# Optimization experiments

Hardware: AMD Instinct MI355X
Metric: run time of the kernel (lower is better)

## Reference

```python
import jax, jax.numpy as jnp
import numpy as np

D_MODEL = 256
N_HEADS = 8
B, S = 8, 2048
TEMP = jnp.sqrt(jnp.float32(D_MODEL))  # ScaledDotProductAttention(temperature=d_model) -> sqrt(d_model)
NEG = jnp.float32(-1e9)


def setup_inputs() -> dict:
    key = jax.random.key(0)
    ks = jax.random.split(key, 12)
    dh = D_MODEL * N_HEADS
    sc_in = 1.0 / np.sqrt(D_MODEL)
    sc_out = 1.0 / np.sqrt(dh)
    return {
        "query": jax.random.normal(ks[0], (B, S, D_MODEL), jnp.float32),
        "key": jax.random.normal(ks[1], (B, S, D_MODEL), jnp.float32),
        "value": jax.random.normal(ks[2], (B, S, D_MODEL), jnp.float32),
        "mask": jax.random.bernoulli(ks[3], 0.9, (B, S)),
        "Wq": jax.random.normal(ks[4], (D_MODEL, dh), jnp.float32) * sc_in,
        "bq": jnp.zeros((dh,), jnp.float32),
        "Wk": jax.random.normal(ks[5], (D_MODEL, dh), jnp.float32) * sc_in,
        "bk": jnp.zeros((dh,), jnp.float32),
        "Wv": jax.random.normal(ks[6], (D_MODEL, dh), jnp.float32) * sc_in,
        "bv": jnp.zeros((dh,), jnp.float32),
        "Wo": jax.random.normal(ks[7], (dh, D_MODEL), jnp.float32) * sc_out,
        "bo": jnp.zeros((D_MODEL,), jnp.float32),
    }


def reference(query, key, value, mask, Wq, bq, Wk, bk, Wv, bv, Wo, bo):
    nb = query.shape[0]
    # projections: (B,S,d) @ (d, d*H) -> view (B,S,H,d)
    q = (query @ Wq + bq).reshape(nb, -1, N_HEADS, D_MODEL)
    k = (key @ Wk + bk).reshape(nb, -1, N_HEADS, D_MODEL)
    v = (value @ Wv + bv).reshape(nb, -1, N_HEADS, D_MODEL)
    # torch.matmul on (B,S,H,d): batched over (B,S) -> per-position HxH attention
    attn = jnp.einsum('bshd,bsgd->bshg', q, k) / TEMP
    m = mask[:, :, None, None]  # (B,S,1,1) broadcast, as in mask.view(B,-1,1,1)
    attn = jnp.where(m, attn, NEG)
    attn = jax.nn.softmax(attn, axis=-1)  # dropout p=0 -> identity
    x = jnp.einsum('bshg,bsgd->bshd', attn, v)  # (B,S,H,d)
    # x.transpose(1,2).contiguous().view(B,-1,d*H)
    x = jnp.transpose(x, (0, 2, 1, 3)).reshape(nb, -1, D_MODEL * N_HEADS)
    return x @ Wo + bo
```

## Files before the change

kernel.cpp:

```cpp
#include <hip/hip_runtime.h>
#include <hip/hip_bf16.h>

typedef __hip_bfloat16 bf16;
typedef short bf16x8 __attribute__((ext_vector_type(8)));
typedef float f32x4 __attribute__((ext_vector_type(4)));

#define MFMA16(a,b,c) __builtin_amdgcn_mfma_f32_16x16x32_bf16(a,b,c,0,0,0)

__device__ __forceinline__ unsigned short f2us(float x){
    union{__hip_bfloat16 h; unsigned short u;} c; c.h = __float2bfloat16(x); return c.u;
}
__device__ __forceinline__ float us2f(unsigned short u){
    union{unsigned short u; __hip_bfloat16 h;} c; c.u = u; return __bfloat162float(c.h);
}
__device__ __forceinline__ uint4 pack8(float4 a, float4 b){
    union{unsigned short us[8]; uint4 v;} p;
    p.us[0]=f2us(a.x); p.us[1]=f2us(a.y); p.us[2]=f2us(a.z); p.us[3]=f2us(a.w);
    p.us[4]=f2us(b.x); p.us[5]=f2us(b.y); p.us[6]=f2us(b.z); p.us[7]=f2us(b.w);
    return p.v;
}

__global__ __launch_bounds__(256) void prep_kernel(
    const float* __restrict__ Wq, const float* __restrict__ Wk,
    const float* __restrict__ Wv, const float* __restrict__ bq,
    const float* __restrict__ bk, const float* __restrict__ bv,
    const float* __restrict__ Wo,
    bf16* __restrict__ WqT, bf16* __restrict__ WkT, bf16* __restrict__ WvT,
    float* __restrict__ bqp, float* __restrict__ bkp, float* __restrict__ bvp,
    bf16* __restrict__ WoT)
{
    __shared__ float T[64][68];
    const int tid = threadIdx.x, bx = blockIdx.x;
    if (bx < 384) {
        const int mat = bx / 128, rem = bx % 128;
        const int c0 = (rem >> 5) * 64, n0 = (rem & 31) * 64;
        const float* W = (mat == 0) ? Wq : (mat == 1) ? Wk : Wv;
        bf16* WT = (mat == 0) ? WqT : (mat == 1) ? WkT : WvT;
        #pragma unroll
        for (int it = 0; it < 4; ++it) {
            int pp = tid + (it << 8);
            int cl = pp >> 4, n4 = (pp & 15) * 4;
            float4 f = *(const float4*)(W + (size_t)(c0 + cl) * 2048 + n0 + n4);
            T[cl][n4] = f.x; T[cl][n4+1] = f.y; T[cl][n4+2] = f.z; T[cl][n4+3] = f.w;
        }
        __syncthreads();
        const int h = n0 >> 8, d0 = n0 & 255;
        #pragma unroll
        for (int it = 0; it < 2; ++it) {
            int pp = tid + (it << 8);
            int j = pp >> 3, g = pp & 7;
            union{unsigned short us[8]; uint4 v;} pk;
            #pragma unroll
            for (int u = 0; u < 8; ++u) pk.us[u] = f2us(T[g*8+u][j]);
            *(uint4*)(WT + (size_t)((d0 + j) * 8 + h) * 256 + c0 + g * 8) = pk.v;
        }
    } else if (bx < 387) {
        const int mat = bx - 384;
        const float* src = (mat == 0) ? bq : (mat == 1) ? bk : bv;
        float* dst = (mat == 0) ? bqp : (mat == 1) ? bkp : bvp;
        for (int n = tid; n < 2048; n += 256)
            dst[(n & 255) * 8 + (n >> 8)] = src[n];
    } else {
        const int idx = bx - 387;
        const int k0 = (idx >> 2) * 64, c0 = (idx & 3) * 64;
        #pragma unroll
        for (int it = 0; it < 4; ++it) {
            int pp = tid + (it << 8);
            int kl = pp >> 4, c4 = (pp & 15) * 4;
            float4 f = *(const float4*)(Wo + (size_t)(k0 + kl) * 256 + c0 + c4);
            T[kl][c4] = f.x; T[kl][c4+1] = f.y; T[kl][c4+2] = f.z; T[kl][c4+3] = f.w;
        }
        __syncthreads();
        #pragma unroll
        for (int it = 0; it < 2; ++it) {
            int pp = tid + (it << 8);
            int j = pp >> 3, g = pp & 7;
            union{unsigned short us[8]; uint4 v;} pk;
            #pragma unroll
            for (int u = 0; u < 8; ++u) pk.us[u] = f2us(T[g*8+u][j]);
            *(uint4*)(WoT + (size_t)(c0 + j) * 2048 + k0 + g * 8) = pk.v;
        }
    }
}

__global__ __launch_bounds__(512, 2) void qkav_kernel(
    const float* __restrict__ Qin, const float* __restrict__ Kin,
    const float* __restrict__ Vin, const int* __restrict__ mask,
    const bf16* __restrict__ WqT, const bf16* __restrict__ WkT,
    const bf16* __restrict__ WvT,
    const float* __restrict__ bqp, const float* __restrict__ bkp,
    const float* __restrict__ bvp,
    const bf16* __restrict__ WoT, const float* __restrict__ bo,
    float* __restrict__ Out)
{
    __shared__ __align__(16) char smem[147456];
    char* const Xq = smem;
    char* const Xk = smem + 32768;
    char* const QT = smem + 65536;
    char* const KT = smem + 106496;
    float* const RED  = (float*)smem;
    float* const WLDS = (float*)(smem + 106496);
    char* const Xv  = smem;
    char* const VT0 = smem + 32768;
    char* const VT1 = smem + 50176;
    char* const xS0 = smem + 67584;
    char* const xS1 = smem + 83968;

    const int tid  = threadIdx.x;
    const int wid  = tid >> 6, lane = tid & 63;
    const int quad = lane >> 4, l15 = lane & 15;
    const int tok0 = blockIdx.x * 64;
    const int t6   = tid & 63, dg = tid >> 6;

    #pragma unroll
    for (int it = 0; it < 4; ++it) {
        int pp = tid + (it << 9);
        int row = pp >> 5, g = pp & 31;
        const float* s = Qin + (size_t)(tok0 + row) * 256 + g * 8;
        *(uint4*)(Xq + row * 512 + ((g ^ (row & 7)) << 4)) =
            pack8(*(const float4*)s, *(const float4*)(s + 4));
        s = Kin + (size_t)(tok0 + row) * 256 + g * 8;
        *(uint4*)(Xk + row * 512 + ((g ^ (row & 7)) << 4)) =
            pack8(*(const float4*)s, *(const float4*)(s + 4));
    }
    __syncthreads();

    f32x4 sacc[4];
    #pragma unroll
    for (int p = 0; p < 4; ++p)
        #pragma unroll
        for (int i = 0; i < 4; ++i) sacc[p][i] = 0.f;

    for (int Cp = 0; Cp < 8; ++Cp) {
        f32x4 accq[4][2], acck[4][2];
        #pragma unroll
        for (int mt = 0; mt < 4; ++mt)
            #pragma unroll
            for (int nt = 0; nt < 2; ++nt)
                #pragma unroll
                for (int i = 0; i < 4; ++i) { accq[mt][nt][i] = 0.f; acck[mt][nt][i] = 0.f; }
        #pragma unroll
        for (int Ks = 0; Ks < 8; ++Ks) {
            bf16x8 bq[2], bk[2];
            #pragma unroll
            for (int nt = 0; nt < 2; ++nt) {
                const size_t boff =
                    (size_t)(Cp * 256 + wid * 32 + nt * 16 + l15) * 256 + Ks * 32 + quad * 8;
                bq[nt] = *(const bf16x8*)(WqT + boff);
                bk[nt] = *(const bf16x8*)(WkT + boff);
            }
            #pragma unroll
            for (int mt = 0; mt < 4; ++mt) {
                int row = mt * 16 + l15;
                int G = (Ks * 4 + quad) ^ (row & 7);
                bf16x8 aq = *(const bf16x8*)(Xq + row * 512 + (G << 4));
                bf16x8 ak = *(const bf16x8*)(Xk + row * 512 + (G << 4));
                #pragma unroll
                for (int nt = 0; nt < 2; ++nt) {
                    accq[mt][nt] = MFMA16(aq, bq[nt], accq[mt][nt]);
                    acck[mt][nt] = MFMA16(ak, bk[nt], acck[mt][nt]);
                }
            }
        }
        #pragma unroll
        for (int nt = 0; nt < 2; ++nt) {
            const int p2 = wid * 32 + nt * 16 + l15;
            const int rowoff = p2 * 160 + ((p2 >> 6) & 3) * 8;
            const float biq = bqp[Cp * 256 + p2];
            const float bik = bkp[Cp * 256 + p2];
            #pragma unroll
            for (int mt = 0; mt < 4; ++mt) {
                int t0 = mt * 16 + quad * 4;
                union{unsigned short us[4]; uint2 v;} pq, pk;
                #pragma unroll
                for (int i = 0; i < 4; ++i) {
                    pq.us[i] = f2us(accq[mt][nt][i] + biq);
                    pk.us[i] = f2us(acck[mt][nt][i] + bik);
                }
                *(uint2*)(QT + rowoff + t0 * 2) = pq.v;
                *(uint2*)(KT + rowoff + t0 * 2) = pk.v;
            }
        }
        __syncthreads();
        #pragma unroll
        for (int pp2 = 0; pp2 < 4; ++pp2) {
            int tq = 2 * (wid * 4 + pp2) + (l15 >> 3);
            union{unsigned short us[8]; bf16x8 v;} Aq, Bk;
            #pragma unroll
            for (int j = 0; j < 8; ++j) {
                int p2 = (quad * 8 + j) * 8 + (l15 & 7);
                int off = p2 * 160 + ((p2 >> 6) & 3) * 8 + tq * 2;
                Aq.us[j] = *(const unsigned short*)(QT + off);
                Bk.us[j] = *(const unsigned short*)(KT + off);
            }
            sacc[pp2] = MFMA16(Aq.v, Bk.v, sacc[pp2]);
        }
        __syncthreads();
    }

    if ((quad >> 1) == (l15 >> 3)) {
        #pragma unroll
        for (int pp2 = 0; pp2 < 4; ++pp2) {
            int tl = (wid * 4 + pp2) * 2 + (l15 >> 3);
            #pragma unroll
            for (int i = 0; i < 4; ++i)
                RED[tl * 68 + ((quad & 1) * 4 + i) * 8 + (l15 & 7)] = sacc[pp2][i];
        }
    }
    __syncthreads();
    {
        const int tl = tid >> 3, hh = tid & 7;
        const int mk = mask[tok0 + tl];
        const float* r = RED + tl * 68 + hh * 8;
        float m = r[0];
        #pragma unroll
        for (int g = 1; g < 8; ++g) m = fmaxf(m, r[g]);
        float e[8], sum = 0.f;
        #pragma unroll
        for (int g = 0; g < 8; ++g) { e[g] = __expf((r[g] - m) * 0.0625f); sum += e[g]; }
        float inv = 1.f / sum;
        float o[8];
        #pragma unroll
        for (int g = 0; g < 8; ++g) o[g] = mk ? e[g] * inv : 0.125f;
        float* wp = WLDS + tl * 68 + hh * 8;
        *(float4*)wp = make_float4(o[0], o[1], o[2], o[3]);
        *(float4*)(wp + 4) = make_float4(o[4], o[5], o[6], o[7]);
    }
    __syncthreads();

    float wv[64];
    {
        const float* wl = WLDS + t6 * 68;
        #pragma unroll
        for (int i = 0; i < 16; ++i) {
            float4 f = *(const float4*)(wl + i * 4);
            wv[i*4] = f.x; wv[i*4+1] = f.y; wv[i*4+2] = f.z; wv[i*4+3] = f.w;
        }
    }
    #pragma unroll
    for (int it = 0; it < 4; ++it) {
        int pp = tid + (it << 9);
        int row = pp >> 5, g = pp & 31;
        const float* s = Vin + (size_t)(tok0 + row) * 256 + g * 8;
        *(uint4*)(Xv + row * 512 + ((g ^ (row & 7)) << 4)) =
            pack8(*(const float4*)s, *(const float4*)(s + 4));
    }
    __syncthreads();

    const int pll = wid * 16 + l15;

    f32x4 oacc[4][2];
    #pragma unroll
    for (int mt = 0; mt < 4; ++mt)
        #pragma unroll
        for (int nt = 0; nt < 2; ++nt)
            #pragma unroll
            for (int i = 0; i < 4; ++i) oacc[mt][nt][i] = 0.f;

    for (int p = 0; p < 18; ++p) {
        char* const VTw = (p & 1) ? VT1 : VT0;
        char* const VTr = (p & 1) ? VT0 : VT1;
        char* const xSw = (p & 1) ? xS0 : xS1;
        char* const xSr = (p & 1) ? xS1 : xS0;

        if (p < 16) {
            const int C = p;
            f32x4 acc[4];
            #pragma unroll
            for (int mt = 0; mt < 4; ++mt)
                #pragma unroll
                for (int i = 0; i < 4; ++i) acc[mt][i] = 0.f;
            #pragma unroll
            for (int Ks = 0; Ks < 8; ++Ks) {
                bf16x8 b = *(const bf16x8*)(WvT + (size_t)(C * 128 + pll) * 256 + Ks * 32 + quad * 8);
                #pragma unroll
                for (int mt = 0; mt < 4; ++mt) {
                    int row = mt * 16 + l15;
                    int G = (Ks * 4 + quad) ^ (row & 7);
                    bf16x8 a = *(const bf16x8*)(Xv + row * 512 + (G << 4));
                    acc[mt] = MFMA16(a, b, acc[mt]);
                }
            }
            const float biv = bvp[C * 128 + pll];
            #pragma unroll
            for (int mt = 0; mt < 4; ++mt) {
                int t0 = mt * 16 + quad * 4;
                union{unsigned short us[4]; uint2 v;} pk;
                #pragma unroll
                for (int i = 0; i < 4; ++i) pk.us[i] = f2us(acc[mt][i] + biv);
                *(uint2*)(VTw + pll * 136 + t0 * 2) = pk.v;
            }
        }

        if (p >= 1 && p <= 16) {
            #pragma unroll
            for (int dd = 0; dd < 2; ++dd) {
                int d = dg * 2 + dd;
                float vv[8];
                #pragma unroll
                for (int g = 0; g < 8; ++g)
                    vv[g] = us2f(*(const unsigned short*)(VTr + (d * 8 + g) * 136 + t6 * 2));
                #pragma unroll
                for (int h = 0; h < 8; ++h) {
                    float x = 0.f;
                    #pragma unroll
                    for (int g = 0; g < 8; ++g) x = fmaf(wv[h * 8 + g], vv[g], x);
                    int u = (h * 2 + (d >> 3)) ^ (t6 & 15);
                    *(unsigned short*)(xSw + t6 * 256 + u * 16 + (d & 7) * 2) = f2us(x);
                }
            }
        }

        if (p >= 2) {
            const int C = p - 2;
            #pragma unroll
            for (int m = 0; m < 4; ++m) {
                const int j  = 2 * m + (quad >> 1);
                const int k0 = j * 256 + C * 16 + (quad & 1) * 8;
                bf16x8 bfr[2];
                #pragma unroll
                for (int nt = 0; nt < 2; ++nt) {
                    int c = wid * 32 + nt * 16 + l15;
                    bfr[nt] = *(const bf16x8*)(WoT + (size_t)c * 2048 + k0);
                }
                #pragma unroll
                for (int mt = 0; mt < 4; ++mt) {
                    int h = mt * 2 + (l15 >> 3);
                    int t = (l15 & 7) * 8 + j;
                    int u = (h * 2 + (quad & 1)) ^ (t & 15);
                    bf16x8 afr = *(const bf16x8*)(xSr + t * 256 + u * 16);
                    #pragma unroll
                    for (int nt = 0; nt < 2; ++nt)
                        oacc[mt][nt] = MFMA16(afr, bfr[nt], oacc[mt][nt]);
                }
            }
        }

        __syncthreads();
    }

    const int b = tok0 >> 11, sg0 = (tok0 & 2047) >> 3;
    #pragma unroll
    for (int nt = 0; nt < 2; ++nt) {
        int c = wid * 32 + nt * 16 + l15;
        float bias = bo[c];
        #pragma unroll
        for (int mt = 0; mt < 4; ++mt) {
            #pragma unroll
            for (int i = 0; i < 4; ++i) {
                int rr = mt * 16 + quad * 4 + i;
                int h = rr >> 3, sgl = rr & 7;
                size_t r = ((size_t)b << 11) + h * 256 + sg0 + sgl;
                Out[r * 256 + c] = oacc[mt][nt][i] + bias;
            }
        }
    }
}

extern "C" void kernel_launch(void* const* d_in, const int* in_sizes, int n_in,
                              void* d_out, int out_size, void* d_ws, size_t ws_size,
                              hipStream_t stream) {
    const float* query = (const float*)d_in[0];
    const float* key   = (const float*)d_in[1];
    const float* value = (const float*)d_in[2];
    const int*   mask  = (const int*)  d_in[3];
    const float* Wq = (const float*)d_in[4];  const float* bq = (const float*)d_in[5];
    const float* Wk = (const float*)d_in[6];  const float* bk = (const float*)d_in[7];
    const float* Wv = (const float*)d_in[8];  const float* bv = (const float*)d_in[9];
    const float* Wo = (const float*)d_in[10]; const float* bo = (const float*)d_in[11];

    char* ws = (char*)d_ws;
    bf16*  WoT = (bf16*)ws;
    bf16*  WqT = (bf16*)(ws + 1048576);
    bf16*  WkT = (bf16*)(ws + 2097152);
    bf16*  WvT = (bf16*)(ws + 3145728);
    float* bqp = (float*)(ws + 4194304);
    float* bkp = (float*)(ws + 4202496);
    float* bvp = (float*)(ws + 4210688);

    prep_kernel<<<515, 256, 0, stream>>>(
        Wq, Wk, Wv, bq, bk, bv, Wo, WqT, WkT, WvT, bqp, bkp, bvp, WoT);
    qkav_kernel<<<256, 512, 0, stream>>>(
        query, key, value, mask, WqT, WkT, WvT, bqp, bkp, bvp, WoT, bo,
        (float*)d_out);
}
```

Measured before the change: 262.7 us.

## Prefetch next-chunk weight fragments and V input into registers; use lightweight barriers

Software-prefetches the first three K-slices of the Wq/Wk and Wv weight fragments for the next chunk into registers while the current chunk computes. The V input loads are issued early, before the softmax phase, to hide global latency. __syncthreads is replaced with an inline-asm barrier that only waits on LDS counters, so outstanding global loads are not drained at each barrier. This adds register pressure (extra bf16x8 and float4 arrays), which may reduce occupancy or cause spills.

```diff
diff --git a/kernel.cpp b/kernel.cpp
--- a/kernel.cpp
+++ b/kernel.cpp
@@ -6,6 +6,8 @@
 typedef float f32x4 __attribute__((ext_vector_type(4)));
 
 #define MFMA16(a,b,c) __builtin_amdgcn_mfma_f32_16x16x32_bf16(a,b,c,0,0,0)
+
+#define BARRIER() asm volatile("s_waitcnt lgkmcnt(0)\n\ts_barrier" ::: "memory")
 
 __device__ __forceinline__ unsigned short f2us(float x){
     union{__hip_bfloat16 h; unsigned short u;} c; c.h = __float2bfloat16(x); return c.u;
@@ -112,6 +114,17 @@
     const int tok0 = blockIdx.x * 64;
     const int t6   = tid & 63, dg = tid >> 6;
 
+    bf16x8 pbq[2][3], pbk[2][3];
+    #pragma unroll
+    for (int nt = 0; nt < 2; ++nt)
+        #pragma unroll
+        for (int Ks = 0; Ks < 3; ++Ks) {
+            const size_t boff =
+                (size_t)(wid * 32 + nt * 16 + l15) * 256 + Ks * 32 + quad * 8;
+            pbq[nt][Ks] = *(const bf16x8*)(WqT + boff);
+            pbk[nt][Ks] = *(const bf16x8*)(WkT + boff);
+        }
+
     #pragma unroll
     for (int it = 0; it < 4; ++it) {
         int pp = tid + (it << 9);
@@ -123,7 +136,7 @@
         *(uint4*)(Xk + row * 512 + ((g ^ (row & 7)) << 4)) =
             pack8(*(const float4*)s, *(const float4*)(s + 4));
     }
-    __syncthreads();
+    BARRIER();
 
     f32x4 sacc[4];
     #pragma unroll
@@ -144,10 +157,15 @@
             bf16x8 bq[2], bk[2];
             #pragma unroll
             for (int nt = 0; nt < 2; ++nt) {
-                const size_t boff =
-                    (size_t)(Cp * 256 + wid * 32 + nt * 16 + l15) * 256 + Ks * 32 + quad * 8;
-                bq[nt] = *(const bf16x8*)(WqT + boff);
-                bk[nt] = *(const bf16x8*)(WkT + boff);
+                if (Ks < 3) {
+                    bq[nt] = pbq[nt][Ks];
+                    bk[nt] = pbk[nt][Ks];
+                } else {
+                    const size_t boff =
+                        (size_t)(Cp * 256 + wid * 32 + nt * 16 + l15) * 256 + Ks * 32 + quad * 8;
+                    bq[nt] = *(const bf16x8*)(WqT + boff);
+                    bk[nt] = *(const bf16x8*)(WkT + boff);
+                }
             }
             #pragma unroll
             for (int mt = 0; mt < 4; ++mt) {
@@ -162,6 +180,17 @@
                 }
             }
         }
+        if (Cp < 7) {
+            #pragma unroll
+            for (int nt = 0; nt < 2; ++nt)
+                #pragma unroll
+                for (int Ks = 0; Ks < 3; ++Ks) {
+                    const size_t boff =
+                        (size_t)((Cp + 1) * 256 + wid * 32 + nt * 16 + l15) * 256 + Ks * 32 + quad * 8;
+                    pbq[nt][Ks] = *(const bf16x8*)(WqT + boff);
+                    pbk[nt][Ks] = *(const bf16x8*)(WkT + boff);
+                }
+        }
         #pragma unroll
         for (int nt = 0; nt < 2; ++nt) {
             const int p2 = wid * 32 + nt * 16 + l15;
@@ -181,7 +210,7 @@
                 *(uint2*)(KT + rowoff + t0 * 2) = pk.v;
             }
         }
-        __syncthreads();
+        BARRIER();
         #pragma unroll
         for (int pp2 = 0; pp2 < 4; ++pp2) {
             int tq = 2 * (wid * 4 + pp2) + (l15 >> 3);
@@ -195,8 +224,23 @@
             }
             sacc[pp2] = MFMA16(Aq.v, Bk.v, sacc[pp2]);
         }
-        __syncthreads();
-    }
+        BARRIER();
+    }
+
+    float4 xvA[4], xvB[4];
+    #pragma unroll
+    for (int it = 0; it < 4; ++it) {
+        int pp = tid + (it << 9);
+        int row = pp >> 5, g = pp & 31;
+        const float* s = Vin + (size_t)(tok0 + row) * 256 + g * 8;
+        xvA[it] = *(const float4*)s;
+        xvB[it] = *(const float4*)(s + 4);
+    }
+    const int pll = wid * 16 + l15;
+    bf16x8 pv[3];
+    #pragma unroll
+    for (int Ks = 0; Ks < 3; ++Ks)
+        pv[Ks] = *(const bf16x8*)(WvT + (size_t)pll * 256 + Ks * 32 + quad * 8);
 
     if ((quad >> 1) == (l15 >> 3)) {
         #pragma unroll
@@ -207,7 +251,7 @@
                 RED[tl * 68 + ((quad & 1) * 4 + i) * 8 + (l15 & 7)] = sacc[pp2][i];
         }
     }
-    __syncthreads();
+    BARRIER();
     {
         const int tl = tid >> 3, hh = tid & 7;
         const int mk = mask[tok0 + tl];
@@ -226,7 +270,7 @@
         *(float4*)wp = make_float4(o[0], o[1], o[2], o[3]);
         *(float4*)(wp + 4) = make_float4(o[4], o[5], o[6], o[7]);
     }
-    __syncthreads();
+    BARRIER();
 
     float wv[64];
     {
@@ -241,13 +285,9 @@
     for (int it = 0; it < 4; ++it) {
         int pp = tid + (it << 9);
         int row = pp >> 5, g = pp & 31;
-        const float* s = Vin + (size_t)(tok0 + row) * 256 + g * 8;
-        *(uint4*)(Xv + row * 512 + ((g ^ (row & 7)) << 4)) =
-            pack8(*(const float4*)s, *(const float4*)(s + 4));
-    }
-    __syncthreads();
-
-    const int pll = wid * 16 + l15;
+        *(uint4*)(Xv + row * 512 + ((g ^ (row & 7)) << 4)) = pack8(xvA[it], xvB[it]);
+    }
+    BARRIER();
 
     f32x4 oacc[4][2];
     #pragma unroll
@@ -272,7 +312,9 @@
                 for (int i = 0; i < 4; ++i) acc[mt][i] = 0.f;
             #pragma unroll
             for (int Ks = 0; Ks < 8; ++Ks) {
-                bf16x8 b = *(const bf16x8*)(WvT + (size_t)(C * 128 + pll) * 256 + Ks * 32 + quad * 8);
+                bf16x8 b;
+                if (Ks < 3) b = pv[Ks];
+                else b = *(const bf16x8*)(WvT + (size_t)(C * 128 + pll) * 256 + Ks * 32 + quad * 8);
                 #pragma unroll
                 for (int mt = 0; mt < 4; ++mt) {
                     int row = mt * 16 + l15;
@@ -280,6 +322,11 @@
                     bf16x8 a = *(const bf16x8*)(Xv + row * 512 + (G << 4));
                     acc[mt] = MFMA16(a, b, acc[mt]);
                 }
+            }
+            if (C < 15) {
+                #pragma unroll
+                for (int Ks = 0; Ks < 3; ++Ks)
+                    pv[Ks] = *(const bf16x8*)(WvT + (size_t)((C + 1) * 128 + pll) * 256 + Ks * 32 + quad * 8);
             }
             const float biv = bvp[C * 128 + pll];
             #pragma unroll
@@ -336,7 +383,7 @@
             }
         }
 
-        __syncthreads();
+        BARRIER();
     }
 
     const int b = tok0 >> 11, sg0 = (tok0 & 2047) >> 3;
```

Measured after the change: 260.6 us. No clear change (-0.8%).

## Fuse weight prep into main kernel with grid-wide atomic barrier

Applied to the files above, without the earlier changes.

Merges the weight transpose/convert prep kernel into the main attention kernel. Each of the 256 blocks first handles up to three prep tiles, then all blocks wait on a global atomic counter barrier before starting the main compute. This removes one kernel launch and the gap between launches, but adds a memset, a spin-wait grid barrier that assumes all 256 blocks are co-resident, and per-block serial prep work done at 512 threads.

```diff
diff --git a/kernel.cpp b/kernel.cpp
--- a/kernel.cpp
+++ b/kernel.cpp
@@ -20,80 +20,90 @@
     return p.v;
 }
 
-__global__ __launch_bounds__(256) void prep_kernel(
-    const float* __restrict__ Wq, const float* __restrict__ Wk,
-    const float* __restrict__ Wv, const float* __restrict__ bq,
-    const float* __restrict__ bk, const float* __restrict__ bv,
-    const float* __restrict__ Wo,
+__global__ __launch_bounds__(512, 2) void fused_kernel(
+    const float* __restrict__ Qin, const float* __restrict__ Kin,
+    const float* __restrict__ Vin, const int* __restrict__ mask,
+    const float* __restrict__ Wq, const float* __restrict__ bq,
+    const float* __restrict__ Wk, const float* __restrict__ bk,
+    const float* __restrict__ Wv, const float* __restrict__ bv,
+    const float* __restrict__ Wo, const float* __restrict__ bo,
     bf16* __restrict__ WqT, bf16* __restrict__ WkT, bf16* __restrict__ WvT,
     float* __restrict__ bqp, float* __restrict__ bkp, float* __restrict__ bvp,
-    bf16* __restrict__ WoT)
-{
-    __shared__ float T[64][68];
-    const int tid = threadIdx.x, bx = blockIdx.x;
-    if (bx < 384) {
-        const int mat = bx / 128, rem = bx % 128;
-        const int c0 = (rem >> 5) * 64, n0 = (rem & 31) * 64;
-        const float* W = (mat == 0) ? Wq : (mat == 1) ? Wk : Wv;
-        bf16* WT = (mat == 0) ? WqT : (mat == 1) ? WkT : WvT;
-        #pragma unroll
-        for (int it = 0; it < 4; ++it) {
-            int pp = tid + (it << 8);
-            int cl = pp >> 4, n4 = (pp & 15) * 4;
-            float4 f = *(const float4*)(W + (size_t)(c0 + cl) * 2048 + n0 + n4);
-            T[cl][n4] = f.x; T[cl][n4+1] = f.y; T[cl][n4+2] = f.z; T[cl][n4+3] = f.w;
-        }
-        __syncthreads();
-        const int h = n0 >> 8, d0 = n0 & 255;
-        #pragma unroll
-        for (int it = 0; it < 2; ++it) {
-            int pp = tid + (it << 8);
-            int j = pp >> 3, g = pp & 7;
-            union{unsigned short us[8]; uint4 v;} pk;
-            #pragma unroll
-            for (int u = 0; u < 8; ++u) pk.us[u] = f2us(T[g*8+u][j]);
-            *(uint4*)(WT + (size_t)((d0 + j) * 8 + h) * 256 + c0 + g * 8) = pk.v;
-        }
-    } else if (bx < 387) {
-        const int mat = bx - 384;
-        const float* src = (mat == 0) ? bq : (mat == 1) ? bk : bv;
-        float* dst = (mat == 0) ? bqp : (mat == 1) ? bkp : bvp;
-        for (int n = tid; n < 2048; n += 256)
-            dst[(n & 255) * 8 + (n >> 8)] = src[n];
-    } else {
-        const int idx = bx - 387;
-        const int k0 = (idx >> 2) * 64, c0 = (idx & 3) * 64;
-        #pragma unroll
-        for (int it = 0; it < 4; ++it) {
-            int pp = tid + (it << 8);
-            int kl = pp >> 4, c4 = (pp & 15) * 4;
-            float4 f = *(const float4*)(Wo + (size_t)(k0 + kl) * 256 + c0 + c4);
-            T[kl][c4] = f.x; T[kl][c4+1] = f.y; T[kl][c4+2] = f.z; T[kl][c4+3] = f.w;
-        }
-        __syncthreads();
-        #pragma unroll
-        for (int it = 0; it < 2; ++it) {
-            int pp = tid + (it << 8);
-            int j = pp >> 3, g = pp & 7;
-            union{unsigned short us[8]; uint4 v;} pk;
-            #pragma unroll
-            for (int u = 0; u < 8; ++u) pk.us[u] = f2us(T[g*8+u][j]);
-            *(uint4*)(WoT + (size_t)(c0 + j) * 2048 + k0 + g * 8) = pk.v;
-        }
-    }
-}
-
-__global__ __launch_bounds__(512, 2) void qkav_kernel(
-    const float* __restrict__ Qin, const float* __restrict__ Kin,
-    const float* __restrict__ Vin, const int* __restrict__ mask,
-    const bf16* __restrict__ WqT, const bf16* __restrict__ WkT,
-    const bf16* __restrict__ WvT,
-    const float* __restrict__ bqp, const float* __restrict__ bkp,
-    const float* __restrict__ bvp,
-    const bf16* __restrict__ WoT, const float* __restrict__ bo,
+    bf16* __restrict__ WoT, unsigned int* __restrict__ cnt,
     float* __restrict__ Out)
 {
     __shared__ __align__(16) char smem[147456];
+    const int tid = threadIdx.x;
+    const int bx  = blockIdx.x;
+
+    {
+        float (*T)[68] = (float (*)[68])smem;
+        #pragma unroll 1
+        for (int ui = 0; ui < 3; ++ui) {
+            if (ui == 2 && bx >= 3) break;
+            const int u = bx + (ui << 8);
+            if (u < 384) {
+                const int mat = u / 128, rem = u % 128;
+                const int c0 = (rem >> 5) * 64, n0 = (rem & 31) * 64;
+                const float* W = (mat == 0) ? Wq : (mat == 1) ? Wk : Wv;
+                bf16* WT = (mat == 0) ? WqT : (mat == 1) ? WkT : WvT;
+                #pragma unroll
+                for (int it = 0; it < 2; ++it) {
+                    int pp = tid + (it << 9);
+                    int cl = pp >> 4, n4 = (pp & 15) * 4;
+                    float4 f = *(const float4*)(W + (size_t)(c0 + cl) * 2048 + n0 + n4);
+                    T[cl][n4] = f.x; T[cl][n4+1] = f.y; T[cl][n4+2] = f.z; T[cl][n4+3] = f.w;
+                }
+                __syncthreads();
+                const int h = n0 >> 8, d0 = n0 & 255;
+                {
+                    int j = tid >> 3, g = tid & 7;
+                    union{unsigned short us[8]; uint4 v;} pk;
+                    #pragma unroll
+                    for (int u2 = 0; u2 < 8; ++u2) pk.us[u2] = f2us(T[g*8+u2][j]);
+                    *(uint4*)(WT + (size_t)((d0 + j) * 8 + h) * 256 + c0 + g * 8) = pk.v;
+                }
+                __syncthreads();
+            } else if (u < 387) {
+                const int mat = u - 384;
+                const float* src = (mat == 0) ? bq : (mat == 1) ? bk : bv;
+                float* dst = (mat == 0) ? bqp : (mat == 1) ? bkp : bvp;
+                for (int n = tid; n < 2048; n += 512)
+                    dst[(n & 255) * 8 + (n >> 8)] = src[n];
+                __syncthreads();
+            } else {
+                const int idx = u - 387;
+                const int k0 = (idx >> 2) * 64, c0 = (idx & 3) * 64;
+                #pragma unroll
+                for (int it = 0; it < 2; ++it) {
+                    int pp = tid + (it << 9);
+                    int kl = pp >> 4, c4 = (pp & 15) * 4;
+                    float4 f = *(const float4*)(Wo + (size_t)(k0 + kl) * 256 + c0 + c4);
+                    T[kl][c4] = f.x; T[kl][c4+1] = f.y; T[kl][c4+2] = f.z; T[kl][c4+3] = f.w;
+                }
+                __syncthreads();
+                {
+                    int j = tid >> 3, g = tid & 7;
+                    union{unsigned short us[8]; uint4 v;} pk;
+                    #pragma unroll
+                    for (int u2 = 0; u2 < 8; ++u2) pk.us[u2] = f2us(T[g*8+u2][j]);
+                    *(uint4*)(WoT + (size_t)(c0 + j) * 2048 + k0 + g * 8) = pk.v;
+                }
+                __syncthreads();
+            }
+        }
+    }
+
+    __syncthreads();
+    if (tid == 0) {
+        __threadfence();
+        __hip_atomic_fetch_add(cnt, 1u, __ATOMIC_RELEASE, __HIP_MEMORY_SCOPE_AGENT);
+        while (__hip_atomic_load(cnt, __ATOMIC_ACQUIRE, __HIP_MEMORY_SCOPE_AGENT) < 256u)
+            __builtin_amdgcn_s_sleep(8);
+        __threadfence();
+    }
+    __syncthreads();
+
     char* const Xq = smem;
     char* const Xk = smem + 32768;
     char* const QT = smem + 65536;
@@ -106,10 +116,9 @@
     char* const xS0 = smem + 67584;
     char* const xS1 = smem + 83968;
 
-    const int tid  = threadIdx.x;
     const int wid  = tid >> 6, lane = tid & 63;
     const int quad = lane >> 4, l15 = lane & 15;
-    const int tok0 = blockIdx.x * 64;
+    const int tok0 = bx * 64;
     const int t6   = tid & 63, dg = tid >> 6;
 
     #pragma unroll
@@ -141,13 +150,13 @@
                 for (int i = 0; i < 4; ++i) { accq[mt][nt][i] = 0.f; acck[mt][nt][i] = 0.f; }
         #pragma unroll
         for (int Ks = 0; Ks < 8; ++Ks) {
-            bf16x8 bq[2], bk[2];
+            bf16x8 bqf[2], bkf[2];
             #pragma unroll
             for (int nt = 0; nt < 2; ++nt) {
                 const size_t boff =
                     (size_t)(Cp * 256 + wid * 32 + nt * 16 + l15) * 256 + Ks * 32 + quad * 8;
-                bq[nt] = *(const bf16x8*)(WqT + boff);
-                bk[nt] = *(const bf16x8*)(WkT + boff);
+                bqf[nt] = *(const bf16x8*)(WqT + boff);
+                bkf[nt] = *(const bf16x8*)(WkT + boff);
             }
             #pragma unroll
             for (int mt = 0; mt < 4; ++mt) {
@@ -157,8 +166,8 @@
                 bf16x8 ak = *(const bf16x8*)(Xk + row * 512 + (G << 4));
                 #pragma unroll
                 for (int nt = 0; nt < 2; ++nt) {
-                    accq[mt][nt] = MFMA16(aq, bq[nt], accq[mt][nt]);
-                    acck[mt][nt] = MFMA16(ak, bk[nt], acck[mt][nt]);
+                    accq[mt][nt] = MFMA16(aq, bqf[nt], accq[mt][nt]);
+                    acck[mt][nt] = MFMA16(ak, bkf[nt], acck[mt][nt]);
                 }
             }
         }
@@ -377,10 +386,10 @@
     float* bqp = (float*)(ws + 4194304);
     float* bkp = (float*)(ws + 4202496);
     float* bvp = (float*)(ws + 4210688);
-
-    prep_kernel<<<515, 256, 0, stream>>>(
-        Wq, Wk, Wv, bq, bk, bv, Wo, WqT, WkT, WvT, bqp, bkp, bvp, WoT);
-    qkav_kernel<<<256, 512, 0, stream>>>(
-        query, key, value, mask, WqT, WkT, WvT, bqp, bkp, bvp, WoT, bo,
-        (float*)d_out);
-}
+    unsigned int* cnt = (unsigned int*)(ws + 4218880);
+
+    hipMemsetAsync(cnt, 0, 16, stream);
+    fused_kernel<<<256, 512, 0, stream>>>(
+        query, key, value, mask, Wq, bq, Wk, bk, Wv, bv, Wo, bo,
+        WqT, WkT, WvT, bqp, bkp, bvp, WoT, cnt, (float*)d_out);
+}
```

New measurement: 293.7 us. 11.8% more time.
